# Kernel tuning notes

Hardware: AMD Instinct MI355X
Metric: run time of the kernel (lower is better)

The kernel has to match this reference:

```python
import jax, jax.numpy as jnp
import numpy as np

VP, B, C, H, W = 8, 2, 512, 16, 16
N_HEAD = 8


def setup_inputs() -> dict:
    key = jax.random.key(0)
    k0, k1, k2, k3, k4 = jax.random.split(key, 5)
    x = jax.random.normal(k0, (VP, B, C, H, W), dtype=jnp.float32)
    s = 1.0 / np.sqrt(C)
    Wqkv = jax.random.normal(k1, (C, 3 * C), dtype=jnp.float32) * s
    bqkv = jnp.zeros((3 * C,), dtype=jnp.float32)
    Wo = jax.random.normal(k2, (C, C), dtype=jnp.float32) * s
    bo = jnp.zeros((C,), dtype=jnp.float32)
    return {"x": x, "Wqkv": Wqkv, "bqkv": bqkv, "Wo": Wo, "bo": bo}


def reference(x, Wqkv, bqkv, Wo, bo):
    vp, b, c, h, w = x.shape
    hw = h * w
    T = vp * hw
    hd = c // N_HEAD
    # 'v b c h w -> b (v h w) c'
    xs = jnp.transpose(x, (1, 0, 3, 4, 2)).reshape(b, T, c)
    qkv = xs @ Wqkv + bqkv  # [b, T, 3c]
    q, k, v = jnp.split(qkv, 3, axis=-1)
    def heads(t):
        return jnp.transpose(t.reshape(b, T, N_HEAD, hd), (0, 2, 1, 3))  # [b, nh, T, hd]
    q, k, v = heads(q), heads(k), heads(v)
    scale = 1.0 / np.sqrt(hd)
    att = jnp.einsum('bhqd,bhkd->bhqk', q, k) * scale  # [b, nh, T, T]
    # block-causal mask: token in block i attends to all tokens in blocks 0..i
    blk = jnp.arange(T) // hw
    allowed = blk[None, :] <= blk[:, None]  # [T, T]
    att = jnp.where(allowed, att, -jnp.inf)
    att = jax.nn.softmax(att, axis=-1)
    y = jnp.einsum('bhqk,bhkd->bhqd', att, v)  # [b, nh, T, hd]
    y = jnp.transpose(y, (0, 2, 1, 3)).reshape(b, T, c)
    y = y @ Wo + bo
    # 'b (v h w) c -> v b c h w'
    y = jnp.transpose(y.reshape(b, vp, h, w, c), (1, 0, 4, 2, 3))
    return y
```

## Files before the change

### kernel.cpp

```cpp
#include <hip/hip_runtime.h>
#include <hip/hip_bf16.h>
#include <stdint.h>

#define VPn 8
#define BBn 2
#define CCn 512
#define NHn 8
#define HDn 64
#define Tn  2048
#define Mn  4096
#define N1n 1536
#define Kn  512
#define QSC 0.180336880111120425f

typedef __attribute__((ext_vector_type(8))) short bf16x8;
typedef __attribute__((ext_vector_type(4))) short s16x4;
typedef __attribute__((ext_vector_type(4))) float f32x4;
typedef __attribute__((ext_vector_type(16))) float f32x16;
typedef __attribute__((ext_vector_type(2))) unsigned int u32x2;
typedef unsigned short u16;
typedef unsigned int   u32;

__device__ __forceinline__ u16 f2bf(float f) {
  return __builtin_bit_cast(u16, __float2bfloat16(f));
}
__device__ __forceinline__ u32 cvtpk(float lo, float hi) {
  u32 r;
  asm("v_cvt_pk_bf16_f32 %0, %1, %2" : "=v"(r) : "v"(lo), "v"(hi));
  return r;
}
__device__ __forceinline__ void gload16(const void* g, void* l) {
  __builtin_amdgcn_global_load_lds(
      (const __attribute__((address_space(1))) u32*)g,
      (__attribute__((address_space(3))) u32*)l, 16, 0, 0);
}

__global__ __launch_bounds__(256) void conv_x(const float* __restrict__ x, u16* __restrict__ A) {
  int bi = blockIdx.x;
  int vb = bi >> 5;
  int ct = (bi >> 2) & 7;
  int ht = bi & 3;
  int v = vb >> 1, b = vb & 1;
  __shared__ float t[64][65];
  int tid = threadIdx.x, col = tid & 63, r4 = tid >> 6;
  const float* src = x + ((size_t)vb * CCn + ct * 64) * 256 + ht * 64;
#pragma unroll
  for (int i = 0; i < 16; ++i) {
    int row = i * 4 + r4;
    t[row][col] = src[row * 256 + col];
  }
  __syncthreads();
  u16* dst = A + ((size_t)(b * Tn + v * 256 + ht * 64)) * Kn + ct * 64;
#pragma unroll
  for (int i = 0; i < 16; ++i) {
    int row = i * 4 + r4;
    dst[row * Kn + col] = f2bf(t[col][row]);
  }
}

__global__ __launch_bounds__(256) void convw(const float* __restrict__ Wqkv, const float* __restrict__ Wo,
                                             u16* __restrict__ WqkvT, u16* __restrict__ WoT) {
  int bi = blockIdx.x;
  const float* Win; u16* Wt; int Cc, rt, ct;
  if (bi < 192) { Win = Wqkv; Wt = WqkvT; Cc = N1n; rt = bi / 24; ct = bi % 24; }
  else { bi -= 192; Win = Wo; Wt = WoT; Cc = CCn; rt = bi / 8; ct = bi % 8; }
  __shared__ float t[64][65];
  int tid = threadIdx.x, col = tid & 63, r4 = tid >> 6;
  const float* src = Win + (size_t)(rt * 64) * Cc + ct * 64;
#pragma unroll
  for (int i = 0; i < 16; ++i) {
    int row = i * 4 + r4;
    t[row][col] = src[row * Cc + col];
  }
  __syncthreads();
  u16* dst = Wt + (size_t)(ct * 64) * Kn + rt * 64;
#pragma unroll
  for (int i = 0; i < 16; ++i) {
    int row = i * 4 + r4;
    dst[row * Kn + col] = f2bf(t[col][row]);
  }
}


__global__ __launch_bounds__(256, 3) void gemm_qkv(
    const u16* __restrict__ A, const u16* __restrict__ Bt, const float* __restrict__ bias,
    u16* __restrict__ Qo, u16* __restrict__ Kp, u16* __restrict__ Vp) {
  const int nt = N1n / 128;
  int m0 = (blockIdx.x / nt) * 64;
  int n0 = (blockIdx.x % nt) * 128;
  __shared__ __align__(16) u16 As[2][64 * 64];
  __shared__ __align__(16) u16 Bs[2][128 * 64];
  int tid = threadIdx.x, lane = tid & 63, w = tid >> 6;
  int wr = w & 1, wc = w >> 1;
  int li = lane & 15, g = lane >> 4;
  int rsub = lane >> 3, slot = lane & 7;
  int srcslot = slot ^ rsub;
  f32x4 acc[2][4] = {};

#define QKV_STAGE(buf, kk0)                                                    \
  {                                                                            \
    _Pragma("unroll")                                                          \
    for (int i = 0; i < 2; ++i) {                                              \
      int ci = w * 2 + i;                                                      \
      int row = ci * 8 + rsub;                                                 \
      gload16(A + (size_t)(m0 + row) * Kn + (kk0) + srcslot * 8,               \
              (char*)&As[buf][0] + ci * 1024);                                 \
    }                                                                          \
    _Pragma("unroll")                                                          \
    for (int i = 0; i < 4; ++i) {                                              \
      int ci = w * 4 + i;                                                      \
      int row = ci * 8 + rsub;                                                 \
      gload16(Bt + (size_t)(n0 + row) * Kn + (kk0) + srcslot * 8,              \
              (char*)&Bs[buf][0] + ci * 1024);                                 \
    }                                                                          \
  }

  QKV_STAGE(0, 0);
#pragma unroll
  for (int step = 0; step < 8; ++step) {
    const int cur = step & 1;
    if (step < 7) {
      QKV_STAGE(cur ^ 1, (step + 1) * 64);
      asm volatile("s_waitcnt vmcnt(6)");
    } else {
      asm volatile("s_waitcnt vmcnt(0)");
    }
    __builtin_amdgcn_s_barrier();
#pragma unroll
    for (int kk = 0; kk < 2; ++kk) {
      bf16x8 af[2], bfr[4];
#pragma unroll
      for (int mi = 0; mi < 2; ++mi) {
        int row = wr * 32 + mi * 16 + li;
        int sw = ((kk * 4 + g) ^ (row & 7)) * 8;
        af[mi] = *(const bf16x8*)(&As[cur][0] + row * 64 + sw);
      }
#pragma unroll
      for (int ni = 0; ni < 4; ++ni) {
        int row = wc * 64 + ni * 16 + li;
        int sw = ((kk * 4 + g) ^ (row & 7)) * 8;
        bfr[ni] = *(const bf16x8*)(&Bs[cur][0] + row * 64 + sw);
      }
#pragma unroll
      for (int mi = 0; mi < 2; ++mi)
#pragma unroll
        for (int ni = 0; ni < 4; ++ni)
          acc[mi][ni] = __builtin_amdgcn_mfma_f32_16x16x32_bf16(af[mi], bfr[ni], acc[mi][ni], 0, 0, 0);
    }
    asm volatile("s_waitcnt lgkmcnt(0)");
    __builtin_amdgcn_sched_barrier(0);
    __builtin_amdgcn_s_barrier();
  }
#pragma unroll
  for (int ni = 0; ni < 4; ++ni) {
    int n = n0 + wc * 64 + ni * 16 + li;
    float bn = bias[n];
    int sel = n >> 9, c = n & 511, hh = c >> 6, d = c & 63;
    if (sel == 0) {
#pragma unroll
      for (int mi = 0; mi < 2; ++mi) {
#pragma unroll
        for (int r = 0; r < 4; ++r) {
          int m = m0 + wr * 32 + mi * 16 + g * 4 + r;
          int bq = m >> 11, t = m & 2047;
          Qo[((size_t)((bq * NHn + hh) * Tn + t)) * HDn + d] = f2bf((acc[mi][ni][r] + bn) * QSC);
        }
      }
    } else if (sel == 1) {
      int kc = d >> 4, khi = (d >> 3) & 1, kj = d & 7;
#pragma unroll
      for (int mi = 0; mi < 2; ++mi) {
#pragma unroll
        for (int r = 0; r < 4; ++r) {
          int m = m0 + wr * 32 + mi * 16 + g * 4 + r;
          int bq = m >> 11, t = m & 2047;
          size_t off = (size_t)(bq * NHn + hh) * 131072 + (size_t)(t >> 5) * 2048 +
                       kc * 512 + khi * 256 + (t & 31) * 8 + kj;
          Kp[off] = f2bf(acc[mi][ni][r] + bn);
        }
      }
    } else {
      int dh = d >> 5, lqd = d & 31;
#pragma unroll
      for (int mi = 0; mi < 2; ++mi) {
        int mb = m0 + wr * 32 + mi * 16 + g * 4;
        int bq = mb >> 11, t0 = mb & 2047;
        size_t off = (size_t)(bq * NHn + hh) * 131072 + (size_t)(t0 >> 5) * 2048 +
                     dh * 1024 + ((t0 >> 4) & 1) * 512 + lqd * 16 +
                     ((t0 >> 2) & 1) * 8 + ((t0 >> 3) & 1) * 4;
        u32x2 ov;
        ov.x = cvtpk(acc[mi][ni][0] + bn, acc[mi][ni][1] + bn);
        ov.y = cvtpk(acc[mi][ni][2] + bn, acc[mi][ni][3] + bn);
        *(u32x2*)(Vp + off) = ov;
      }
    }
  }
}

__global__ __launch_bounds__(256, 4) void attn(
    const u16* __restrict__ Q, const u16* __restrict__ Kp, const u16* __restrict__ Vp,
    u16* __restrict__ Y) {
  int idx = blockIdx.x;
  int bh = (idx & 7) | (((idx >> 3) & 1) << 3);
  int qt = 63 - (idx >> 4);
  int b = bh >> 3, h = bh & 7;
  int qrow0 = qt << 5;
  int nkeys = ((qt >> 3) + 1) << 8;
  int qtr = nkeys >> 2;
  int tid = threadIdx.x;
  int w = tid >> 6;
  int kbeg = w * qtr, kend = kbeg + qtr;
  int lane = tid & 63;
  int lq = lane & 31;
  int hi = lane >> 5;

  const u16* Qb = Q + ((size_t)(bh * Tn + qrow0)) * HDn;
  const u16* Kb = Kp + (size_t)bh * 131072;
  const u16* Vb = Vp + (size_t)bh * 131072;
  int kof = hi * 256 + lq * 8;
  int vof = lq * 16 + hi * 8;

  bf16x8 qf[4];
  {
    const u16* qp = Qb + (size_t)lq * HDn + hi * 8;
#pragma unroll
    for (int c = 0; c < 4; ++c) qf[c] = *(const bf16x8*)(qp + c * 16);
  }

  float mrun = -1e30f, lrun = 0.f;
  f32x16 oacc0 = {}, oacc1 = {};

  bf16x8 kc[4];
#pragma unroll
  for (int c = 0; c < 4; ++c)
    kc[c] = *(const bf16x8*)(Kb + (size_t)(kbeg >> 5) * 2048 + c * 512 + kof);

  for (int k0 = kbeg; k0 < kend; k0 += 32) {
    int kt = k0 >> 5;
    int ktn = (k0 + 32 < kend) ? (kt + 1) : kt;
    bf16x8 knf[4];
#pragma unroll
    for (int c = 0; c < 4; ++c)
      knf[c] = *(const bf16x8*)(Kb + (size_t)ktn * 2048 + c * 512 + kof);
    const u16* vt = Vb + (size_t)kt * 2048 + vof;
    bf16x8 va0 = *(const bf16x8*)(vt);
    bf16x8 vb0 = *(const bf16x8*)(vt + 512);
    bf16x8 va1 = *(const bf16x8*)(vt + 1024);
    bf16x8 vb1 = *(const bf16x8*)(vt + 1536);

    f32x16 s = {};
    __builtin_amdgcn_s_setprio(1);
#pragma unroll
    for (int c = 0; c < 4; ++c)
      s = __builtin_amdgcn_mfma_f32_32x32x16_bf16(kc[c], qf[c], s, 0, 0, 0);
    __builtin_amdgcn_s_setprio(0);

    float m0 = fmaxf(fmaxf(fmaxf(fmaxf(s[0], s[1]), fmaxf(s[2], s[3])),
                           fmaxf(fmaxf(s[4], s[5]), fmaxf(s[6], s[7]))),
                     fmaxf(fmaxf(fmaxf(s[8], s[9]), fmaxf(s[10], s[11])),
                           fmaxf(fmaxf(s[12], s[13]), fmaxf(s[14], s[15]))));
    float mall = fmaxf(m0, __shfl_xor(m0, 32));
    if (!__all(mall <= mrun + 8.0f)) {
      float mnew = fmaxf(mrun, mall);
      float fc = exp2f(mrun - mnew);
      mrun = mnew;
      lrun *= fc;
#pragma unroll
      for (int j = 0; j < 16; ++j) { oacc0[j] *= fc; oacc1[j] *= fc; }
    }
    float p[16];
#pragma unroll
    for (int j = 0; j < 16; ++j) p[j] = exp2f(s[j] - mrun);
    lrun += (((p[0] + p[1]) + (p[2] + p[3])) + ((p[4] + p[5]) + (p[6] + p[7]))) +
            (((p[8] + p[9]) + (p[10] + p[11])) + ((p[12] + p[13]) + (p[14] + p[15])));

    bf16x8 pfA, pfB;
    {
      __attribute__((ext_vector_type(4))) int pa = {
          (int)cvtpk(p[0], p[1]), (int)cvtpk(p[2], p[3]),
          (int)cvtpk(p[4], p[5]), (int)cvtpk(p[6], p[7])};
      __attribute__((ext_vector_type(4))) int pb = {
          (int)cvtpk(p[8], p[9]), (int)cvtpk(p[10], p[11]),
          (int)cvtpk(p[12], p[13]), (int)cvtpk(p[14], p[15])};
      pfA = __builtin_bit_cast(bf16x8, pa);
      pfB = __builtin_bit_cast(bf16x8, pb);
    }

    __builtin_amdgcn_s_setprio(1);
    oacc0 = __builtin_amdgcn_mfma_f32_32x32x16_bf16(va0, pfA, oacc0, 0, 0, 0);
    oacc0 = __builtin_amdgcn_mfma_f32_32x32x16_bf16(vb0, pfB, oacc0, 0, 0, 0);
    oacc1 = __builtin_amdgcn_mfma_f32_32x32x16_bf16(va1, pfA, oacc1, 0, 0, 0);
    oacc1 = __builtin_amdgcn_mfma_f32_32x32x16_bf16(vb1, pfB, oacc1, 0, 0, 0);
    __builtin_amdgcn_s_setprio(0);
#pragma unroll
    for (int c = 0; c < 4; ++c) kc[c] = knf[c];
  }

  lrun += __shfl_xor(lrun, 32);

  __shared__ float Ol[4][32][68];
  __shared__ float ml[2][4][32];
  {
    float* op = &Ol[w][lq][hi * 4];
#pragma unroll
    for (int a = 0; a < 4; ++a) {
      f32x4 v0 = {oacc0[4 * a], oacc0[4 * a + 1], oacc0[4 * a + 2], oacc0[4 * a + 3]};
      f32x4 v1 = {oacc1[4 * a], oacc1[4 * a + 1], oacc1[4 * a + 2], oacc1[4 * a + 3]};
      *(f32x4*)(op + a * 8) = v0;
      *(f32x4*)(op + 32 + a * 8) = v1;
    }
    if (lane < 32) { ml[0][w][lq] = mrun; ml[1][w][lq] = lrun; }
  }
  __syncthreads();

#pragma unroll
  for (int task = tid; task < 512; task += 256) {
    int q = task >> 4, quad = task & 15;
    float m0v = ml[0][0][q], m1v = ml[0][1][q], m2v = ml[0][2][q], m3v = ml[0][3][q];
    float mx = fmaxf(fmaxf(m0v, m1v), fmaxf(m2v, m3v));
    float w0 = exp2f(m0v - mx), w1 = exp2f(m1v - mx);
    float w2 = exp2f(m2v - mx), w3 = exp2f(m3v - mx);
    float l = ml[1][0][q] * w0 + ml[1][1][q] * w1 + ml[1][2][q] * w2 + ml[1][3][q] * w3;
    float inv = 1.0f / l;
    f32x4 o0 = *(const f32x4*)&Ol[0][q][quad * 4];
    f32x4 o1 = *(const f32x4*)&Ol[1][q][quad * 4];
    f32x4 o2 = *(const f32x4*)&Ol[2][q][quad * 4];
    f32x4 o3 = *(const f32x4*)&Ol[3][q][quad * 4];
    float y0 = (o0[0] * w0 + o1[0] * w1 + o2[0] * w2 + o3[0] * w3) * inv;
    float y1 = (o0[1] * w0 + o1[1] * w1 + o2[1] * w2 + o3[1] * w3) * inv;
    float y2 = (o0[2] * w0 + o1[2] * w1 + o2[2] * w2 + o3[2] * w3) * inv;
    float y3 = (o0[3] * w0 + o1[3] * w1 + o2[3] * w2 + o3[3] * w3) * inv;
    u32x2 yv;
    yv.x = cvtpk(y0, y1);
    yv.y = cvtpk(y2, y3);
    *(u32x2*)(Y + ((size_t)(b * Tn + qrow0 + q)) * CCn + h * HDn + quad * 4) = yv;
  }
}

__global__ __launch_bounds__(256, 4) void gemm_out(
    const u16* __restrict__ A, const u16* __restrict__ Bt, const float* __restrict__ bias,
    float* __restrict__ out) {
  const int nt = 8;
  int m0 = (blockIdx.x / nt) * 64;
  int n0 = (blockIdx.x % nt) * 64;
  __shared__ __align__(16) u16 As[2][64 * 64];
  __shared__ __align__(16) u16 Bs[2][64 * 64];
  int tid = threadIdx.x, lane = tid & 63, w = tid >> 6;
  int wr = w & 1, wc = w >> 1;
  int li = lane & 15, g = lane >> 4;
  int rsub = lane >> 3, slot = lane & 7;
  int srcslot = slot ^ rsub;
  f32x4 acc[2][2] = {};

#define OUT_STAGE(buf, kk0)                                                    \
  {                                                                            \
    _Pragma("unroll")                                                          \
    for (int i = 0; i < 2; ++i) {                                              \
      int ci = w * 2 + i;                                                      \
      int row = ci * 8 + rsub;                                                 \
      gload16(A + (size_t)(m0 + row) * Kn + (kk0) + srcslot * 8,               \
              (char*)&As[buf][0] + ci * 1024);                                 \
      gload16(Bt + (size_t)(n0 + row) * Kn + (kk0) + srcslot * 8,              \
              (char*)&Bs[buf][0] + ci * 1024);                                 \
    }                                                                          \
  }

  OUT_STAGE(0, 0);
#pragma unroll
  for (int step = 0; step < 8; ++step) {
    const int cur = step & 1;
    if (step < 7) {
      OUT_STAGE(cur ^ 1, (step + 1) * 64);
      asm volatile("s_waitcnt vmcnt(4)");
    } else {
      asm volatile("s_waitcnt vmcnt(0)");
    }
    __builtin_amdgcn_s_barrier();
#pragma unroll
    for (int kk = 0; kk < 2; ++kk) {
      bf16x8 af[2], bfr[2];
#pragma unroll
      for (int mi = 0; mi < 2; ++mi) {
        int row = wr * 32 + mi * 16 + li;
        int sw = ((kk * 4 + g) ^ (row & 7)) * 8;
        af[mi] = *(const bf16x8*)(&As[cur][0] + row * 64 + sw);
      }
#pragma unroll
      for (int ni = 0; ni < 2; ++ni) {
        int row = wc * 32 + ni * 16 + li;
        int sw = ((kk * 4 + g) ^ (row & 7)) * 8;
        bfr[ni] = *(const bf16x8*)(&Bs[cur][0] + row * 64 + sw);
      }
#pragma unroll
      for (int mi = 0; mi < 2; ++mi)
#pragma unroll
        for (int ni = 0; ni < 2; ++ni)
          acc[mi][ni] = __builtin_amdgcn_mfma_f32_16x16x32_bf16(af[mi], bfr[ni], acc[mi][ni], 0, 0, 0);
    }
    asm volatile("s_waitcnt lgkmcnt(0)");
    __builtin_amdgcn_sched_barrier(0);
    __builtin_amdgcn_s_barrier();
  }
  int b = m0 >> 11, v = (m0 >> 8) & 7, hw0 = m0 & 255;
  float* ob = out + (size_t)((v * 2 + b) * 512) * 256;
#pragma unroll
  for (int ni = 0; ni < 2; ++ni) {
    int n = n0 + wc * 32 + ni * 16 + li;
    float bn = bias[n];
#pragma unroll
    for (int mi = 0; mi < 2; ++mi) {
      int hw = hw0 + wr * 32 + mi * 16 + g * 4;
      f32x4 y;
#pragma unroll
      for (int r = 0; r < 4; ++r) y[r] = acc[mi][ni][r] + bn;
      *(f32x4*)(ob + (size_t)n * 256 + hw) = y;
    }
  }
}

extern "C" void kernel_launch(void* const* d_in, const int* in_sizes, int n_in,
                              void* d_out, int out_size, void* d_ws, size_t ws_size,
                              hipStream_t stream) {
  (void)in_sizes; (void)n_in; (void)out_size; (void)ws_size;
  const float* x    = (const float*)d_in[0];
  const float* Wqkv = (const float*)d_in[1];
  const float* bqkv = (const float*)d_in[2];
  const float* Wo   = (const float*)d_in[3];
  const float* bo   = (const float*)d_in[4];
  float* out = (float*)d_out;
  char* ws = (char*)d_ws;
  const size_t MB = 1ull << 20;
  u16*   Abf   = (u16*)(ws + 0);
  u16*   WqkvT = (u16*)(ws + 4 * MB);
  u16*   WoT   = (u16*)(ws + 5 * MB + 512 * 1024);
  u16*   Qb    = (u16*)(ws + 6 * MB);
  u16*   Kb    = (u16*)(ws + 10 * MB);
  u16*   VTb   = (u16*)(ws + 14 * MB);

  conv_x<<<512, 256, 0, stream>>>(x, Abf);
  convw<<<256, 256, 0, stream>>>(Wqkv, Wo, WqkvT, WoT);
  gemm_qkv<<<64 * 12, 256, 0, stream>>>(Abf, WqkvT, bqkv, Qb, Kb, VTb);
  attn<<<1024, 256, 0, stream>>>(Qb, Kb, VTb, Abf);
  gemm_out<<<64 * 8, 256, 0, stream>>>(Abf, WoT, bo, out);
}
```

Measured before the change: 60.54 us.

## Software-pipeline attention PV with next QK, fuse prep kernels, relax launch bounds

```diff
diff --git a/kernel.cpp b/kernel.cpp
--- a/kernel.cpp
+++ b/kernel.cpp
@@ -35,49 +35,50 @@
       (__attribute__((address_space(3))) u32*)l, 16, 0, 0);
 }
 
-__global__ __launch_bounds__(256) void conv_x(const float* __restrict__ x, u16* __restrict__ A) {
+__global__ __launch_bounds__(256) void prep(const float* __restrict__ x,
+                                            const float* __restrict__ Wqkv,
+                                            const float* __restrict__ Wo,
+                                            u16* __restrict__ A,
+                                            u16* __restrict__ WqkvT,
+                                            u16* __restrict__ WoT) {
   int bi = blockIdx.x;
-  int vb = bi >> 5;
-  int ct = (bi >> 2) & 7;
-  int ht = bi & 3;
-  int v = vb >> 1, b = vb & 1;
   __shared__ float t[64][65];
   int tid = threadIdx.x, col = tid & 63, r4 = tid >> 6;
-  const float* src = x + ((size_t)vb * CCn + ct * 64) * 256 + ht * 64;
-#pragma unroll
-  for (int i = 0; i < 16; ++i) {
-    int row = i * 4 + r4;
-    t[row][col] = src[row * 256 + col];
-  }
-  __syncthreads();
-  u16* dst = A + ((size_t)(b * Tn + v * 256 + ht * 64)) * Kn + ct * 64;
-#pragma unroll
-  for (int i = 0; i < 16; ++i) {
-    int row = i * 4 + r4;
-    dst[row * Kn + col] = f2bf(t[col][row]);
-  }
-}
-
-__global__ __launch_bounds__(256) void convw(const float* __restrict__ Wqkv, const float* __restrict__ Wo,
-                                             u16* __restrict__ WqkvT, u16* __restrict__ WoT) {
-  int bi = blockIdx.x;
-  const float* Win; u16* Wt; int Cc, rt, ct;
-  if (bi < 192) { Win = Wqkv; Wt = WqkvT; Cc = N1n; rt = bi / 24; ct = bi % 24; }
-  else { bi -= 192; Win = Wo; Wt = WoT; Cc = CCn; rt = bi / 8; ct = bi % 8; }
-  __shared__ float t[64][65];
-  int tid = threadIdx.x, col = tid & 63, r4 = tid >> 6;
-  const float* src = Win + (size_t)(rt * 64) * Cc + ct * 64;
-#pragma unroll
-  for (int i = 0; i < 16; ++i) {
-    int row = i * 4 + r4;
-    t[row][col] = src[row * Cc + col];
-  }
-  __syncthreads();
-  u16* dst = Wt + (size_t)(ct * 64) * Kn + rt * 64;
-#pragma unroll
-  for (int i = 0; i < 16; ++i) {
-    int row = i * 4 + r4;
-    dst[row * Kn + col] = f2bf(t[col][row]);
+  if (bi < 512) {
+    int vb = bi >> 5;
+    int ct = (bi >> 2) & 7;
+    int ht = bi & 3;
+    int v = vb >> 1, b = vb & 1;
+    const float* src = x + ((size_t)vb * CCn + ct * 64) * 256 + ht * 64;
+#pragma unroll
+    for (int i = 0; i < 16; ++i) {
+      int row = i * 4 + r4;
+      t[row][col] = src[row * 256 + col];
+    }
+    __syncthreads();
+    u16* dst = A + ((size_t)(b * Tn + v * 256 + ht * 64)) * Kn + ct * 64;
+#pragma unroll
+    for (int i = 0; i < 16; ++i) {
+      int row = i * 4 + r4;
+      dst[row * Kn + col] = f2bf(t[col][row]);
+    }
+  } else {
+    const float* Win; u16* Wt; int Cc, rt, ct;
+    if (bi < 704) { int k = bi - 512; Win = Wqkv; Wt = WqkvT; Cc = N1n; rt = k / 24; ct = k % 24; }
+    else          { int k = bi - 704; Win = Wo;   Wt = WoT;   Cc = CCn; rt = k / 8;  ct = k % 8;  }
+    const float* src = Win + (size_t)(rt * 64) * Cc + ct * 64;
+#pragma unroll
+    for (int i = 0; i < 16; ++i) {
+      int row = i * 4 + r4;
+      t[row][col] = src[row * Cc + col];
+    }
+    __syncthreads();
+    u16* dst = Wt + (size_t)(ct * 64) * Kn + rt * 64;
+#pragma unroll
+    for (int i = 0; i < 16; ++i) {
+      int row = i * 4 + r4;
+      dst[row * Kn + col] = f2bf(t[col][row]);
+    }
   }
 }
 
@@ -197,7 +198,7 @@
   }
 }
 
-__global__ __launch_bounds__(256, 4) void attn(
+__global__ __launch_bounds__(256, 3) void attn(
     const u16* __restrict__ Q, const u16* __restrict__ Kp, const u16* __restrict__ Vp,
     u16* __restrict__ Y) {
   int idx = blockIdx.x;
@@ -209,7 +210,8 @@
   int qtr = nkeys >> 2;
   int tid = threadIdx.x;
   int w = tid >> 6;
-  int kbeg = w * qtr, kend = kbeg + qtr;
+  int ktb = (w * qtr) >> 5;
+  int ntile = qtr >> 5;
   int lane = tid & 63;
   int lq = lane & 31;
   int hi = lane >> 5;
@@ -229,72 +231,84 @@
 
   float mrun = -1e30f, lrun = 0.f;
   f32x16 oacc0 = {}, oacc1 = {};
-
-  bf16x8 kc[4];
-#pragma unroll
-  for (int c = 0; c < 4; ++c)
-    kc[c] = *(const bf16x8*)(Kb + (size_t)(kbeg >> 5) * 2048 + c * 512 + kof);
-
-  for (int k0 = kbeg; k0 < kend; k0 += 32) {
-    int kt = k0 >> 5;
-    int ktn = (k0 + 32 < kend) ? (kt + 1) : kt;
-    bf16x8 knf[4];
-#pragma unroll
-    for (int c = 0; c < 4; ++c)
-      knf[c] = *(const bf16x8*)(Kb + (size_t)ktn * 2048 + c * 512 + kof);
-    const u16* vt = Vb + (size_t)kt * 2048 + vof;
-    bf16x8 va0 = *(const bf16x8*)(vt);
-    bf16x8 vb0 = *(const bf16x8*)(vt + 512);
-    bf16x8 va1 = *(const bf16x8*)(vt + 1024);
-    bf16x8 vb1 = *(const bf16x8*)(vt + 1536);
-
+  bf16x8 kc[4], knf[4], vc[4], vn[4];
+  bf16x8 pfA, pfB;
+
+#define KLD(dst, kt)                                                           \
+  _Pragma("unroll")                                                            \
+  for (int c = 0; c < 4; ++c)                                                  \
+    dst[c] = *(const bf16x8*)(Kb + (size_t)(kt) * 2048 + c * 512 + kof);
+#define VLD(dst, kt)                                                           \
+  {                                                                            \
+    const u16* vt_ = Vb + (size_t)(kt) * 2048 + vof;                           \
+    _Pragma("unroll")                                                          \
+    for (int c = 0; c < 4; ++c) dst[c] = *(const bf16x8*)(vt_ + c * 512);      \
+  }
+#define SQK()                                                                  \
+  __builtin_amdgcn_s_setprio(1);                                               \
+  _Pragma("unroll")                                                            \
+  for (int c = 0; c < 4; ++c)                                                  \
+    s = __builtin_amdgcn_mfma_f32_32x32x16_bf16(kc[c], qf[c], s, 0, 0, 0);     \
+  __builtin_amdgcn_s_setprio(0);
+#define PVB()                                                                  \
+  __builtin_amdgcn_s_setprio(1);                                               \
+  oacc0 = __builtin_amdgcn_mfma_f32_32x32x16_bf16(vc[0], pfA, oacc0, 0, 0, 0); \
+  oacc0 = __builtin_amdgcn_mfma_f32_32x32x16_bf16(vc[1], pfB, oacc0, 0, 0, 0); \
+  oacc1 = __builtin_amdgcn_mfma_f32_32x32x16_bf16(vc[2], pfA, oacc1, 0, 0, 0); \
+  oacc1 = __builtin_amdgcn_mfma_f32_32x32x16_bf16(vc[3], pfB, oacc1, 0, 0, 0); \
+  __builtin_amdgcn_s_setprio(0);
+#define SMB()                                                                  \
+  {                                                                            \
+    float m0_ = fmaxf(fmaxf(fmaxf(fmaxf(s[0], s[1]), fmaxf(s[2], s[3])),       \
+                            fmaxf(fmaxf(s[4], s[5]), fmaxf(s[6], s[7]))),      \
+                      fmaxf(fmaxf(fmaxf(s[8], s[9]), fmaxf(s[10], s[11])),     \
+                            fmaxf(fmaxf(s[12], s[13]), fmaxf(s[14], s[15])))); \
+    float mall_ = fmaxf(m0_, __shfl_xor(m0_, 32));                             \
+    if (!__all(mall_ <= mrun + 8.0f)) {                                        \
+      float mnew_ = fmaxf(mrun, mall_);                                        \
+      float fc_ = exp2f(mrun - mnew_);                                         \
+      mrun = mnew_; lrun *= fc_;                                               \
+      _Pragma("unroll")                                                        \
+      for (int j = 0; j < 16; ++j) { oacc0[j] *= fc_; oacc1[j] *= fc_; }       \
+    }                                                                          \
+    float p[16];                                                               \
+    _Pragma("unroll")                                                          \
+    for (int j = 0; j < 16; ++j) p[j] = exp2f(s[j] - mrun);                    \
+    lrun += (((p[0] + p[1]) + (p[2] + p[3])) + ((p[4] + p[5]) + (p[6] + p[7]))) + \
+            (((p[8] + p[9]) + (p[10] + p[11])) + ((p[12] + p[13]) + (p[14] + p[15]))); \
+    __attribute__((ext_vector_type(4))) int pa_ = {                            \
+        (int)cvtpk(p[0], p[1]), (int)cvtpk(p[2], p[3]),                        \
+        (int)cvtpk(p[4], p[5]), (int)cvtpk(p[6], p[7])};                       \
+    __attribute__((ext_vector_type(4))) int pb_ = {                            \
+        (int)cvtpk(p[8], p[9]), (int)cvtpk(p[10], p[11]),                      \
+        (int)cvtpk(p[12], p[13]), (int)cvtpk(p[14], p[15])};                   \
+    pfA = __builtin_bit_cast(bf16x8, pa_);                                     \
+    pfB = __builtin_bit_cast(bf16x8, pb_);                                     \
+  }
+
+  KLD(kc, ktb);
+  VLD(vc, ktb);
+  KLD(knf, ktb + 1);
+  {
     f32x16 s = {};
-    __builtin_amdgcn_s_setprio(1);
-#pragma unroll
-    for (int c = 0; c < 4; ++c)
-      s = __builtin_amdgcn_mfma_f32_32x32x16_bf16(kc[c], qf[c], s, 0, 0, 0);
-    __builtin_amdgcn_s_setprio(0);
-
-    float m0 = fmaxf(fmaxf(fmaxf(fmaxf(s[0], s[1]), fmaxf(s[2], s[3])),
-                           fmaxf(fmaxf(s[4], s[5]), fmaxf(s[6], s[7]))),
-                     fmaxf(fmaxf(fmaxf(s[8], s[9]), fmaxf(s[10], s[11])),
-                           fmaxf(fmaxf(s[12], s[13]), fmaxf(s[14], s[15]))));
-    float mall = fmaxf(m0, __shfl_xor(m0, 32));
-    if (!__all(mall <= mrun + 8.0f)) {
-      float mnew = fmaxf(mrun, mall);
-      float fc = exp2f(mrun - mnew);
-      mrun = mnew;
-      lrun *= fc;
-#pragma unroll
-      for (int j = 0; j < 16; ++j) { oacc0[j] *= fc; oacc1[j] *= fc; }
-    }
-    float p[16];
-#pragma unroll
-    for (int j = 0; j < 16; ++j) p[j] = exp2f(s[j] - mrun);
-    lrun += (((p[0] + p[1]) + (p[2] + p[3])) + ((p[4] + p[5]) + (p[6] + p[7]))) +
-            (((p[8] + p[9]) + (p[10] + p[11])) + ((p[12] + p[13]) + (p[14] + p[15])));
-
-    bf16x8 pfA, pfB;
-    {
-      __attribute__((ext_vector_type(4))) int pa = {
-          (int)cvtpk(p[0], p[1]), (int)cvtpk(p[2], p[3]),
-          (int)cvtpk(p[4], p[5]), (int)cvtpk(p[6], p[7])};
-      __attribute__((ext_vector_type(4))) int pb = {
-          (int)cvtpk(p[8], p[9]), (int)cvtpk(p[10], p[11]),
-          (int)cvtpk(p[12], p[13]), (int)cvtpk(p[14], p[15])};
-      pfA = __builtin_bit_cast(bf16x8, pa);
-      pfB = __builtin_bit_cast(bf16x8, pb);
-    }
-
-    __builtin_amdgcn_s_setprio(1);
-    oacc0 = __builtin_amdgcn_mfma_f32_32x32x16_bf16(va0, pfA, oacc0, 0, 0, 0);
-    oacc0 = __builtin_amdgcn_mfma_f32_32x32x16_bf16(vb0, pfB, oacc0, 0, 0, 0);
-    oacc1 = __builtin_amdgcn_mfma_f32_32x32x16_bf16(va1, pfA, oacc1, 0, 0, 0);
-    oacc1 = __builtin_amdgcn_mfma_f32_32x32x16_bf16(vb1, pfB, oacc1, 0, 0, 0);
-    __builtin_amdgcn_s_setprio(0);
-#pragma unroll
-    for (int c = 0; c < 4; ++c) kc[c] = knf[c];
-  }
+    SQK();
+    SMB();
+  }
+#pragma unroll
+  for (int c = 0; c < 4; ++c) kc[c] = knf[c];
+
+  for (int t = 1; t < ntile; ++t) {
+    int ktn = ktb + ((t + 1 < ntile) ? t + 1 : t);
+    KLD(knf, ktn);
+    VLD(vn, ktb + t);
+    f32x16 s = {};
+    SQK();
+    PVB();
+    SMB();
+#pragma unroll
+    for (int c = 0; c < 4; ++c) { kc[c] = knf[c]; vc[c] = vn[c]; }
+  }
+  PVB();
 
   lrun += __shfl_xor(lrun, 32);
 
@@ -437,8 +451,7 @@
   u16*   Kb    = (u16*)(ws + 10 * MB);
   u16*   VTb   = (u16*)(ws + 14 * MB);
 
-  conv_x<<<512, 256, 0, stream>>>(x, Abf);
-  convw<<<256, 256, 0, stream>>>(Wqkv, Wo, WqkvT, WoT);
+  prep<<<768, 256, 0, stream>>>(x, Wqkv, Wo, Abf, WqkvT, WoT);
   gemm_qkv<<<64 * 12, 256, 0, stream>>>(Abf, WqkvT, bqkv, Qb, Kb, VTb);
   attn<<<1024, 256, 0, stream>>>(Qb, Kb, VTb, Abf);
   gemm_out<<<64 * 8, 256, 0, stream>>>(Abf, WoT, bo, out);
```

After: 57.62 us (median of 3 runs). 1.05x faster.

## Share LDS-staged K/V tiles across two query tiles in attention; merge prep kernels

Applied to the files above, without the earlier changes.

```diff
diff --git a/kernel.cpp b/kernel.cpp
--- a/kernel.cpp
+++ b/kernel.cpp
@@ -35,49 +35,50 @@
       (__attribute__((address_space(3))) u32*)l, 16, 0, 0);
 }
 
-__global__ __launch_bounds__(256) void conv_x(const float* __restrict__ x, u16* __restrict__ A) {
+__global__ __launch_bounds__(256) void prep(const float* __restrict__ x,
+                                            const float* __restrict__ Wqkv,
+                                            const float* __restrict__ Wo,
+                                            u16* __restrict__ A,
+                                            u16* __restrict__ WqkvT,
+                                            u16* __restrict__ WoT) {
   int bi = blockIdx.x;
-  int vb = bi >> 5;
-  int ct = (bi >> 2) & 7;
-  int ht = bi & 3;
-  int v = vb >> 1, b = vb & 1;
   __shared__ float t[64][65];
   int tid = threadIdx.x, col = tid & 63, r4 = tid >> 6;
-  const float* src = x + ((size_t)vb * CCn + ct * 64) * 256 + ht * 64;
-#pragma unroll
-  for (int i = 0; i < 16; ++i) {
-    int row = i * 4 + r4;
-    t[row][col] = src[row * 256 + col];
-  }
-  __syncthreads();
-  u16* dst = A + ((size_t)(b * Tn + v * 256 + ht * 64)) * Kn + ct * 64;
-#pragma unroll
-  for (int i = 0; i < 16; ++i) {
-    int row = i * 4 + r4;
-    dst[row * Kn + col] = f2bf(t[col][row]);
-  }
-}
-
-__global__ __launch_bounds__(256) void convw(const float* __restrict__ Wqkv, const float* __restrict__ Wo,
-                                             u16* __restrict__ WqkvT, u16* __restrict__ WoT) {
-  int bi = blockIdx.x;
-  const float* Win; u16* Wt; int Cc, rt, ct;
-  if (bi < 192) { Win = Wqkv; Wt = WqkvT; Cc = N1n; rt = bi / 24; ct = bi % 24; }
-  else { bi -= 192; Win = Wo; Wt = WoT; Cc = CCn; rt = bi / 8; ct = bi % 8; }
-  __shared__ float t[64][65];
-  int tid = threadIdx.x, col = tid & 63, r4 = tid >> 6;
-  const float* src = Win + (size_t)(rt * 64) * Cc + ct * 64;
-#pragma unroll
-  for (int i = 0; i < 16; ++i) {
-    int row = i * 4 + r4;
-    t[row][col] = src[row * Cc + col];
-  }
-  __syncthreads();
-  u16* dst = Wt + (size_t)(ct * 64) * Kn + rt * 64;
-#pragma unroll
-  for (int i = 0; i < 16; ++i) {
-    int row = i * 4 + r4;
-    dst[row * Kn + col] = f2bf(t[col][row]);
+  if (bi < 512) {
+    int vb = bi >> 5;
+    int ct = (bi >> 2) & 7;
+    int ht = bi & 3;
+    int v = vb >> 1, b = vb & 1;
+    const float* src = x + ((size_t)vb * CCn + ct * 64) * 256 + ht * 64;
+#pragma unroll
+    for (int i = 0; i < 16; ++i) {
+      int row = i * 4 + r4;
+      t[row][col] = src[row * 256 + col];
+    }
+    __syncthreads();
+    u16* dst = A + ((size_t)(b * Tn + v * 256 + ht * 64)) * Kn + ct * 64;
+#pragma unroll
+    for (int i = 0; i < 16; ++i) {
+      int row = i * 4 + r4;
+      dst[row * Kn + col] = f2bf(t[col][row]);
+    }
+  } else {
+    const float* Win; u16* Wt; int Cc, rt, ct;
+    if (bi < 704) { int k = bi - 512; Win = Wqkv; Wt = WqkvT; Cc = N1n; rt = k / 24; ct = k % 24; }
+    else          { int k = bi - 704; Win = Wo;   Wt = WoT;   Cc = CCn; rt = k / 8;  ct = k % 8;  }
+    const float* src = Win + (size_t)(rt * 64) * Cc + ct * 64;
+#pragma unroll
+    for (int i = 0; i < 16; ++i) {
+      int row = i * 4 + r4;
+      t[row][col] = src[row * Cc + col];
+    }
+    __syncthreads();
+    u16* dst = Wt + (size_t)(ct * 64) * Kn + rt * 64;
+#pragma unroll
+    for (int i = 0; i < 16; ++i) {
+      int row = i * 4 + r4;
+      dst[row * Kn + col] = f2bf(t[col][row]);
+    }
   }
 }
 
@@ -197,57 +198,63 @@
   }
 }
 
-__global__ __launch_bounds__(256, 4) void attn(
+__global__ __launch_bounds__(512, 4) void attn(
     const u16* __restrict__ Q, const u16* __restrict__ Kp, const u16* __restrict__ Vp,
     u16* __restrict__ Y) {
   int idx = blockIdx.x;
   int bh = (idx & 7) | (((idx >> 3) & 1) << 3);
-  int qt = 63 - (idx >> 4);
+  int qp = 31 - (idx >> 4);
   int b = bh >> 3, h = bh & 7;
-  int qrow0 = qt << 5;
-  int nkeys = ((qt >> 3) + 1) << 8;
-  int qtr = nkeys >> 2;
+  int nkeys = ((qp >> 2) + 1) << 8;
+  int ntile = nkeys >> 7;
   int tid = threadIdx.x;
   int w = tid >> 6;
-  int kbeg = w * qtr, kend = kbeg + qtr;
+  int seg = w >> 1, jt = w & 1;
+  int tile0 = seg * ntile;
   int lane = tid & 63;
-  int lq = lane & 31;
-  int hi = lane >> 5;
-
-  const u16* Qb = Q + ((size_t)(bh * Tn + qrow0)) * HDn;
+  int lq = lane & 31, hi = lane >> 5;
+
+  const u16* Qb = Q + ((size_t)(bh * Tn + (qp << 6) + jt * 32)) * HDn;
   const u16* Kb = Kp + (size_t)bh * 131072;
   const u16* Vb = Vp + (size_t)bh * 131072;
+  const u16* sbase = (w & 1) ? Vb : Kb;
   int kof = hi * 256 + lq * 8;
   int vof = lq * 16 + hi * 8;
 
+  __shared__ __align__(16) char smem[71680];
+  u16 (*KVs)[2][4][2048] = (u16 (*)[2][4][2048])smem;
+
   bf16x8 qf[4];
   {
-    const u16* qp = Qb + (size_t)lq * HDn + hi * 8;
-#pragma unroll
-    for (int c = 0; c < 4; ++c) qf[c] = *(const bf16x8*)(qp + c * 16);
+    const u16* qptr = Qb + (size_t)lq * HDn + hi * 8;
+#pragma unroll
+    for (int c = 0; c < 4; ++c) qf[c] = *(const bf16x8*)(qptr + c * 16);
   }
 
   float mrun = -1e30f, lrun = 0.f;
   f32x16 oacc0 = {}, oacc1 = {};
 
-  bf16x8 kc[4];
-#pragma unroll
-  for (int c = 0; c < 4; ++c)
-    kc[c] = *(const bf16x8*)(Kb + (size_t)(kbeg >> 5) * 2048 + c * 512 + kof);
-
-  for (int k0 = kbeg; k0 < kend; k0 += 32) {
-    int kt = k0 >> 5;
-    int ktn = (k0 + 32 < kend) ? (kt + 1) : kt;
-    bf16x8 knf[4];
-#pragma unroll
-    for (int c = 0; c < 4; ++c)
-      knf[c] = *(const bf16x8*)(Kb + (size_t)ktn * 2048 + c * 512 + kof);
-    const u16* vt = Vb + (size_t)kt * 2048 + vof;
-    bf16x8 va0 = *(const bf16x8*)(vt);
-    bf16x8 vb0 = *(const bf16x8*)(vt + 512);
-    bf16x8 va1 = *(const bf16x8*)(vt + 1024);
-    bf16x8 vb1 = *(const bf16x8*)(vt + 1536);
-
+#define AST(buf, t)                                                            \
+  {                                                                            \
+    _Pragma("unroll")                                                          \
+    for (int i_ = 0; i_ < 4; ++i_)                                             \
+      gload16(sbase + (size_t)(tile0 + (t)) * 2048 + i_ * 512 + lane * 8,      \
+              &KVs[buf][w & 1][seg][i_ * 512]);                                \
+  }
+
+  AST(0, 0);
+  asm volatile("s_waitcnt vmcnt(0)");
+  __builtin_amdgcn_s_barrier();
+
+  for (int t = 0; t < ntile; ++t) {
+    const int cur = t & 1;
+    if (t + 1 < ntile) { AST(cur ^ 1, t + 1); }
+    bf16x8 kc[4], vc[4];
+#pragma unroll
+    for (int c = 0; c < 4; ++c) {
+      kc[c] = *(const bf16x8*)&KVs[cur][0][seg][c * 512 + kof];
+      vc[c] = *(const bf16x8*)&KVs[cur][1][seg][c * 512 + vof];
+    }
     f32x16 s = {};
     __builtin_amdgcn_s_setprio(1);
 #pragma unroll
@@ -255,11 +262,11 @@
       s = __builtin_amdgcn_mfma_f32_32x32x16_bf16(kc[c], qf[c], s, 0, 0, 0);
     __builtin_amdgcn_s_setprio(0);
 
-    float m0 = fmaxf(fmaxf(fmaxf(fmaxf(s[0], s[1]), fmaxf(s[2], s[3])),
-                           fmaxf(fmaxf(s[4], s[5]), fmaxf(s[6], s[7]))),
-                     fmaxf(fmaxf(fmaxf(s[8], s[9]), fmaxf(s[10], s[11])),
-                           fmaxf(fmaxf(s[12], s[13]), fmaxf(s[14], s[15]))));
-    float mall = fmaxf(m0, __shfl_xor(m0, 32));
+    float m0_ = fmaxf(fmaxf(fmaxf(fmaxf(s[0], s[1]), fmaxf(s[2], s[3])),
+                            fmaxf(fmaxf(s[4], s[5]), fmaxf(s[6], s[7]))),
+                      fmaxf(fmaxf(fmaxf(s[8], s[9]), fmaxf(s[10], s[11])),
+                            fmaxf(fmaxf(s[12], s[13]), fmaxf(s[14], s[15]))));
+    float mall = fmaxf(m0_, __shfl_xor(m0_, 32));
     if (!__all(mall <= mrun + 8.0f)) {
       float mnew = fmaxf(mrun, mall);
       float fc = exp2f(mrun - mnew);
@@ -273,35 +280,35 @@
     for (int j = 0; j < 16; ++j) p[j] = exp2f(s[j] - mrun);
     lrun += (((p[0] + p[1]) + (p[2] + p[3])) + ((p[4] + p[5]) + (p[6] + p[7]))) +
             (((p[8] + p[9]) + (p[10] + p[11])) + ((p[12] + p[13]) + (p[14] + p[15])));
-
     bf16x8 pfA, pfB;
     {
-      __attribute__((ext_vector_type(4))) int pa = {
+      __attribute__((ext_vector_type(4))) int pa_ = {
           (int)cvtpk(p[0], p[1]), (int)cvtpk(p[2], p[3]),
           (int)cvtpk(p[4], p[5]), (int)cvtpk(p[6], p[7])};
-      __attribute__((ext_vector_type(4))) int pb = {
+      __attribute__((ext_vector_type(4))) int pb_ = {
           (int)cvtpk(p[8], p[9]), (int)cvtpk(p[10], p[11]),
           (int)cvtpk(p[12], p[13]), (int)cvtpk(p[14], p[15])};
-      pfA = __builtin_bit_cast(bf16x8, pa);
-      pfB = __builtin_bit_cast(bf16x8, pb);
-    }
-
+      pfA = __builtin_bit_cast(bf16x8, pa_);
+      pfB = __builtin_bit_cast(bf16x8, pb_);
+    }
     __builtin_amdgcn_s_setprio(1);
-    oacc0 = __builtin_amdgcn_mfma_f32_32x32x16_bf16(va0, pfA, oacc0, 0, 0, 0);
-    oacc0 = __builtin_amdgcn_mfma_f32_32x32x16_bf16(vb0, pfB, oacc0, 0, 0, 0);
-    oacc1 = __builtin_amdgcn_mfma_f32_32x32x16_bf16(va1, pfA, oacc1, 0, 0, 0);
-    oacc1 = __builtin_amdgcn_mfma_f32_32x32x16_bf16(vb1, pfB, oacc1, 0, 0, 0);
+    oacc0 = __builtin_amdgcn_mfma_f32_32x32x16_bf16(vc[0], pfA, oacc0, 0, 0, 0);
+    oacc0 = __builtin_amdgcn_mfma_f32_32x32x16_bf16(vc[1], pfB, oacc0, 0, 0, 0);
+    oacc1 = __builtin_amdgcn_mfma_f32_32x32x16_bf16(vc[2], pfA, oacc1, 0, 0, 0);
+    oacc1 = __builtin_amdgcn_mfma_f32_32x32x16_bf16(vc[3], pfB, oacc1, 0, 0, 0);
     __builtin_amdgcn_s_setprio(0);
-#pragma unroll
-    for (int c = 0; c < 4; ++c) kc[c] = knf[c];
+
+    asm volatile("s_waitcnt vmcnt(0)");
+    __builtin_amdgcn_s_barrier();
   }
 
   lrun += __shfl_xor(lrun, 32);
 
-  __shared__ float Ol[4][32][68];
-  __shared__ float ml[2][4][32];
+  __syncthreads();
+  float* OlB = (float*)smem;
+  float* mlB = (float*)(smem + 69632);
   {
-    float* op = &Ol[w][lq][hi * 4];
+    float* op = OlB + (size_t)((jt * 4 + seg) * 32 + lq) * 68 + hi * 4;
 #pragma unroll
     for (int a = 0; a < 4; ++a) {
       f32x4 v0 = {oacc0[4 * a], oacc0[4 * a + 1], oacc0[4 * a + 2], oacc0[4 * a + 3]};
@@ -309,23 +316,33 @@
       *(f32x4*)(op + a * 8) = v0;
       *(f32x4*)(op + 32 + a * 8) = v1;
     }
-    if (lane < 32) { ml[0][w][lq] = mrun; ml[1][w][lq] = lrun; }
+    if (lane < 32) {
+      mlB[((jt * 2 + 0) * 4 + seg) * 32 + lq] = mrun;
+      mlB[((jt * 2 + 1) * 4 + seg) * 32 + lq] = lrun;
+    }
   }
   __syncthreads();
 
-#pragma unroll
-  for (int task = tid; task < 512; task += 256) {
-    int q = task >> 4, quad = task & 15;
-    float m0v = ml[0][0][q], m1v = ml[0][1][q], m2v = ml[0][2][q], m3v = ml[0][3][q];
+  for (int task = tid; task < 1024; task += 512) {
+    int set = task >> 9;
+    int q = (task >> 4) & 31;
+    int quad = task & 15;
+    float m0v = mlB[((set * 2) * 4 + 0) * 32 + q];
+    float m1v = mlB[((set * 2) * 4 + 1) * 32 + q];
+    float m2v = mlB[((set * 2) * 4 + 2) * 32 + q];
+    float m3v = mlB[((set * 2) * 4 + 3) * 32 + q];
     float mx = fmaxf(fmaxf(m0v, m1v), fmaxf(m2v, m3v));
     float w0 = exp2f(m0v - mx), w1 = exp2f(m1v - mx);
     float w2 = exp2f(m2v - mx), w3 = exp2f(m3v - mx);
-    float l = ml[1][0][q] * w0 + ml[1][1][q] * w1 + ml[1][2][q] * w2 + ml[1][3][q] * w3;
+    float l = mlB[((set * 2 + 1) * 4 + 0) * 32 + q] * w0 +
+              mlB[((set * 2 + 1) * 4 + 1) * 32 + q] * w1 +
+              mlB[((set * 2 + 1) * 4 + 2) * 32 + q] * w2 +
+              mlB[((set * 2 + 1) * 4 + 3) * 32 + q] * w3;
     float inv = 1.0f / l;
-    f32x4 o0 = *(const f32x4*)&Ol[0][q][quad * 4];
-    f32x4 o1 = *(const f32x4*)&Ol[1][q][quad * 4];
-    f32x4 o2 = *(const f32x4*)&Ol[2][q][quad * 4];
-    f32x4 o3 = *(const f32x4*)&Ol[3][q][quad * 4];
+    f32x4 o0 = *(const f32x4*)(OlB + (size_t)((set * 4 + 0) * 32 + q) * 68 + quad * 4);
+    f32x4 o1 = *(const f32x4*)(OlB + (size_t)((set * 4 + 1) * 32 + q) * 68 + quad * 4);
+    f32x4 o2 = *(const f32x4*)(OlB + (size_t)((set * 4 + 2) * 32 + q) * 68 + quad * 4);
+    f32x4 o3 = *(const f32x4*)(OlB + (size_t)((set * 4 + 3) * 32 + q) * 68 + quad * 4);
     float y0 = (o0[0] * w0 + o1[0] * w1 + o2[0] * w2 + o3[0] * w3) * inv;
     float y1 = (o0[1] * w0 + o1[1] * w1 + o2[1] * w2 + o3[1] * w3) * inv;
     float y2 = (o0[2] * w0 + o1[2] * w1 + o2[2] * w2 + o3[2] * w3) * inv;
@@ -333,7 +350,7 @@
     u32x2 yv;
     yv.x = cvtpk(y0, y1);
     yv.y = cvtpk(y2, y3);
-    *(u32x2*)(Y + ((size_t)(b * Tn + qrow0 + q)) * CCn + h * HDn + quad * 4) = yv;
+    *(u32x2*)(Y + ((size_t)(b * Tn + (qp << 6) + set * 32 + q)) * CCn + h * HDn + quad * 4) = yv;
   }
 }
 
@@ -437,9 +454,8 @@
   u16*   Kb    = (u16*)(ws + 10 * MB);
   u16*   VTb   = (u16*)(ws + 14 * MB);
 
-  conv_x<<<512, 256, 0, stream>>>(x, Abf);
-  convw<<<256, 256, 0, stream>>>(Wqkv, Wo, WqkvT, WoT);
+  prep<<<768, 256, 0, stream>>>(x, Wqkv, Wo, Abf, WqkvT, WoT);
   gemm_qkv<<<64 * 12, 256, 0, stream>>>(Abf, WqkvT, bqkv, Qb, Kb, VTb);
-  attn<<<1024, 256, 0, stream>>>(Qb, Kb, VTb, Abf);
+  attn<<<512, 512, 0, stream>>>(Qb, Kb, VTb, Abf);
   gemm_out<<<64 * 8, 256, 0, stream>>>(Abf, WoT, bo, out);
 }
```

Measured after the change: 60.67 us. Within noise of the previous version (+0.2%).
